# Optimization experiments

Hardware: AMD Instinct MI355X
Metric: run time of the kernel (lower is better)

Reference implementation:

```python
import jax, jax.numpy as jnp
import numpy as np

N_NODES = 100000
N_EDGES = 1600000
D_IN = 128
D_HID = 128


def _sage_conv(x, edge_index, w_l, b_l, w_r):
    """PyG SAGEConv (aggr='mean'): lin_l(mean_j x_j) + lin_r(x_i).
    lin_l has bias, lin_r does not."""
    src, dst = edge_index[0], edge_index[1]
    n = x.shape[0]
    msgs = x[src]                                   # [E, D] gather
    agg = jax.ops.segment_sum(msgs, dst, num_segments=n)        # [N, D]
    cnt = jax.ops.segment_sum(jnp.ones((src.shape[0], 1), x.dtype), dst,
                              num_segments=n)                   # [N, 1]
    mean = agg / jnp.maximum(cnt, 1.0)
    return mean @ w_l.T + b_l + x @ w_r.T


def setup_inputs() -> dict:
    key = jax.random.key(0)
    ks = jax.random.split(key, 7)
    x = jax.random.normal(ks[0], (N_NODES, D_IN), dtype=jnp.float32)
    edge_index = jax.random.randint(ks[1], (2, N_EDGES), 0, N_NODES, dtype=jnp.int64)
    s = 1.0 / np.sqrt(D_IN)
    w1_l = jax.random.uniform(ks[2], (D_HID, D_IN), jnp.float32, -s, s)
    b1_l = jnp.zeros((D_HID,), jnp.float32)
    w1_r = jax.random.uniform(ks[3], (D_HID, D_IN), jnp.float32, -s, s)
    s2 = 1.0 / np.sqrt(D_HID)
    w2_l = jax.random.uniform(ks[4], (1, D_HID), jnp.float32, -s2, s2)
    b2_l = jnp.zeros((1,), jnp.float32)
    w2_r = jax.random.uniform(ks[5], (1, D_HID), jnp.float32, -s2, s2)
    return {"x": x, "edge_index": edge_index,
            "w1_l": w1_l, "b1_l": b1_l, "w1_r": w1_r,
            "w2_l": w2_l, "b2_l": b2_l, "w2_r": w2_r}


def reference(x, edge_index, w1_l, b1_l, w1_r, w2_l, b2_l, w2_r):
    h = _sage_conv(x, edge_index, w1_l, b1_l, w1_r)          # [N, hidden]
    out = jax.nn.relu(h)
    out = _sage_conv(out, edge_index, w2_l, b2_l, w2_r)      # [N, 1]
    out = jax.nn.sigmoid(out)
    return (out, h)
```

## Files before the change

kernel.cpp:

```cpp
#include <hip/hip_runtime.h>
#include <hip/hip_bf16.h>

#define D   128
#define CAP 64

typedef __bf16 v8bf __attribute__((ext_vector_type(8)));
typedef float  v4f  __attribute__((ext_vector_type(4)));

__device__ __forceinline__ unsigned f2bf(float f) {
    unsigned u = __float_as_uint(f);
    return (u + 0x7fffu + ((u >> 16) & 1u)) >> 16;
}
__device__ __forceinline__ float bf2f_lo(unsigned v) { return __uint_as_float(v << 16); }
__device__ __forceinline__ float bf2f_hi(unsigned v) { return __uint_as_float(v & 0xffff0000u); }

__global__ void detect_k(const unsigned* __restrict__ e32, int sample, int* __restrict__ flag) {
    __shared__ int nz;
    if (threadIdx.x == 0) nz = 0;
    __syncthreads();
    int c = 0;
    for (int j = 0; j < 4; ++j) {
        int i = threadIdx.x * 4 + j;
        if (i < sample && e32[2 * i + 1] != 0u) c++;
    }
    if (c) atomicAdd(&nz, c);
    __syncthreads();
    if (threadIdx.x == 0) *flag = (nz == 0) ? 1 : 0;
}

__device__ __forceinline__ void load_edge(const void* edge, int use64, int E, int e,
                                          int& src, int& dst) {
    if (use64) {
        src = (int)((const long long*)edge)[e];
        dst = (int)((const long long*)edge)[E + e];
    } else {
        src = ((const int*)edge)[e];
        dst = ((const int*)edge)[E + e];
    }
}


__global__ __launch_bounds__(256) void xcast_k(
    const float* __restrict__ x, short* __restrict__ axm, int N)
{
    int gid = blockIdx.x * 256 + threadIdx.x;
    int g = gid >> 6, cp = gid & 63;
    if (g >= N) return;
    float2 v = *(const float2*)&x[(size_t)g * D + cp * 2];
    unsigned packed = f2bf(v.x) | (f2bf(v.y) << 16);
    *(unsigned*)&axm[(size_t)g * 256 + 128 + cp * 2] = packed;
}

__global__ __launch_bounds__(256) void build2_k(
    const void* __restrict__ edge, int* __restrict__ deg,
    int* __restrict__ slots, const int* __restrict__ flag, int E)
{
    int e0 = (blockIdx.x * 256 + threadIdx.x) * 2;
    const int use64 = *flag;
#pragma unroll
    for (int t = 0; t < 2; ++t) {
        int e = e0 + t;
        if (e < E) {
            int src, dst;
            load_edge(edge, use64, E, e, src, dst);
            int c = atomicAdd(&deg[dst], 1);
            if (c < CAP) slots[dst * CAP + c] = src;
        }
    }
}

__global__ __launch_bounds__(256) void agg_bf_k(
    short* axm, const int* __restrict__ slots,
    const int* __restrict__ deg, int N)
{
    int gw = (blockIdx.x * 256 + threadIdx.x) >> 6;
    int lane = threadIdx.x & 63;
    if (gw >= N) return;
    int dg = deg[gw];
    int n = min(dg, CAP);
    const int* sl = &slots[gw * CAP];
    float a0x = 0, a0y = 0, a1x = 0, a1y = 0, a2x = 0, a2y = 0, a3x = 0, a3y = 0;
    int j = 0;
    for (; j + 3 < n; j += 4) {
        int s0 = sl[j], s1 = sl[j + 1], s2 = sl[j + 2], s3 = sl[j + 3];
        unsigned v0 = *(const unsigned*)&axm[(size_t)s0 * 256 + 128 + lane * 2];
        unsigned v1 = *(const unsigned*)&axm[(size_t)s1 * 256 + 128 + lane * 2];
        unsigned v2 = *(const unsigned*)&axm[(size_t)s2 * 256 + 128 + lane * 2];
        unsigned v3 = *(const unsigned*)&axm[(size_t)s3 * 256 + 128 + lane * 2];
        a0x += bf2f_lo(v0); a0y += bf2f_hi(v0);
        a1x += bf2f_lo(v1); a1y += bf2f_hi(v1);
        a2x += bf2f_lo(v2); a2y += bf2f_hi(v2);
        a3x += bf2f_lo(v3); a3y += bf2f_hi(v3);
    }
    for (; j < n; ++j) {
        unsigned v0 = *(const unsigned*)&axm[(size_t)sl[j] * 256 + 128 + lane * 2];
        a0x += bf2f_lo(v0); a0y += bf2f_hi(v0);
    }
    float inv = 1.0f / fmaxf((float)dg, 1.0f);
    float mx = (a0x + a1x + a2x + a3x) * inv;
    float my = (a0y + a1y + a2y + a3y) * inv;
    *(unsigned*)&axm[(size_t)gw * 256 + lane * 2] = f2bf(mx) | (f2bf(my) << 16);
}

__global__ __launch_bounds__(256) void prep_bfrag_k(
    const float* __restrict__ w1l, const float* __restrict__ w1r,
    short* __restrict__ bfrag)
{
    int flat = blockIdx.x * 256 + threadIdx.x;
    int kt = flat >> 9, nt = (flat >> 6) & 7, lane = flat & 63;
    int c  = nt * 16 + (lane & 15);
    int k0 = kt * 32 + (lane >> 4) * 8;
    short out[8];
#pragma unroll
    for (int j = 0; j < 8; ++j) {
        int kk = k0 + j;
        float v = (kk < 128) ? w1l[c * 128 + kk] : w1r[c * 128 + (kk - 128)];
        out[j] = (short)f2bf(v);
    }
    *(uint4*)&bfrag[(size_t)flat * 8] = *(uint4*)out;
}

__global__ __launch_bounds__(256) void gemm_mfma_k(
    const short* axm, const short* __restrict__ bfrag,
    const float* __restrict__ b1,
    const float* __restrict__ w2l, const float* __restrict__ w2r,
    float* h, float* __restrict__ p, float* __restrict__ q, int N)
{
    __shared__ short sA[64 * 256];
    const int tid = threadIdx.x;
    const int row0 = blockIdx.x * 64;

#pragma unroll
    for (int i = 0; i < 8; ++i) {
        int cg = i * 256 + tid;
        int r = cg >> 5, c = cg & 31;
        int g = row0 + r;
        uint4 v = make_uint4(0u, 0u, 0u, 0u);
        if (g < N) v = *(const uint4*)&axm[(size_t)g * 256 + c * 8];
        int lb = r * 512 + ((c * 16) ^ ((r & 7) << 4));
        *(uint4*)((char*)sA + lb) = v;
    }
    __syncthreads();

    const int w    = tid >> 6;
    const int lane = tid & 63;
    const int col  = lane & 15;
    const int kg   = lane >> 4;

    v4f acc[8];
#pragma unroll
    for (int nt = 0; nt < 8; ++nt) {
        float bv = b1[nt * 16 + col];
        acc[nt] = (v4f){bv, bv, bv, bv};
    }

    const int arow  = w * 16 + col;
    const int abase = arow * 512;
    const int axor  = (arow & 7) << 4;

#pragma unroll
    for (int kt = 0; kt < 8; ++kt) {
        int chunk = kt * 4 + kg;
        v8bf a = *(const v8bf*)((const char*)sA + abase + ((chunk * 16) ^ axor));
#pragma unroll
        for (int nt = 0; nt < 8; ++nt) {
            v8bf b = *(const v8bf*)&bfrag[(size_t)(((kt * 8 + nt) << 6) + lane) * 8];
            acc[nt] = __builtin_amdgcn_mfma_f32_16x16x32_bf16(a, b, acc[nt], 0, 0, 0);
        }
    }

    float pp[4] = {0, 0, 0, 0}, qq[4] = {0, 0, 0, 0};
#pragma unroll
    for (int nt = 0; nt < 8; ++nt) {
        float w2lv = w2l[nt * 16 + col];
        float w2rv = w2r[nt * 16 + col];
#pragma unroll
        for (int r = 0; r < 4; ++r) {
            int g = row0 + w * 16 + kg * 4 + r;
            float hv = acc[nt][r];
            if (g < N) h[(size_t)g * D + nt * 16 + col] = hv;
            float rl = fmaxf(hv, 0.f);
            pp[r] += rl * w2lv;
            qq[r] += rl * w2rv;
        }
    }
#pragma unroll
    for (int r = 0; r < 4; ++r) {
#pragma unroll
        for (int m = 8; m >= 1; m >>= 1) {
            pp[r] += __shfl_xor(pp[r], m, 64);
            qq[r] += __shfl_xor(qq[r], m, 64);
        }
    }
    if (col == 0) {
#pragma unroll
        for (int r = 0; r < 4; ++r) {
            int g = row0 + w * 16 + kg * 4 + r;
            if (g < N) { p[g] = pp[r]; q[g] = qq[r]; }
        }
    }
}

__global__ __launch_bounds__(256) void final3_k(
    const float* __restrict__ p, const float* __restrict__ q,
    const int* __restrict__ slots, const int* __restrict__ deg,
    const float* __restrict__ b2, float* __restrict__ out, int N)
{
    int gw = (blockIdx.x * 256 + threadIdx.x) >> 6;
    int lane = threadIdx.x & 63;
    if (gw >= N) return;
    int dg = deg[gw];
    int n = min(dg, CAP);
    float s = 0.f;
    if (lane < n) s = p[slots[gw * CAP + lane]];
#pragma unroll
    for (int m = 32; m >= 1; m >>= 1) s += __shfl_xor(s, m, 64);
    if (lane == 0) {
        float v = s / fmaxf((float)dg, 1.0f) + b2[0] + q[gw];
        out[gw] = 1.0f / (1.0f + expf(-v));
    }
}

__global__ __launch_bounds__(256) void hist_k(
    const void* __restrict__ edge, int* __restrict__ deg,
    const int* __restrict__ flag, int E)
{
    int e = blockIdx.x * 256 + threadIdx.x;
    if (e >= E) return;
    int src, dst;
    load_edge(edge, *flag, E, e, src, dst);
    atomicAdd(&deg[dst], 1);
}

__global__ __launch_bounds__(256) void scan1_k(const int* __restrict__ deg,
                                               int* __restrict__ bsum, int N) {
    __shared__ int ts[256];
    int base = blockIdx.x * 1024;
    int tid = threadIdx.x;
    int s = 0;
#pragma unroll
    for (int j = 0; j < 4; ++j) {
        int i = base + tid * 4 + j;
        if (i < N) s += deg[i];
    }
    ts[tid] = s;
    __syncthreads();
    for (int st = 128; st > 0; st >>= 1) {
        if (tid < st) ts[tid] += ts[tid + st];
        __syncthreads();
    }
    if (tid == 0) bsum[blockIdx.x] = ts[0];
}

__global__ void scan2_k(int* __restrict__ bsum, int nb, int* __restrict__ offsets, int N) {
    if (threadIdx.x == 0 && blockIdx.x == 0) {
        int run = 0;
        for (int b = 0; b < nb; ++b) { int t = bsum[b]; bsum[b] = run; run += t; }
        offsets[N] = run;
    }
}

__global__ __launch_bounds__(256) void scan3_k(
    const int* __restrict__ deg, const int* __restrict__ bsum,
    int* __restrict__ offsets, int* __restrict__ cursor, int N)
{
    __shared__ int ts[256];
    int base = blockIdx.x * 1024;
    int tid = threadIdx.x;
    int v[4];
    int s = 0;
#pragma unroll
    for (int j = 0; j < 4; ++j) {
        int i = base + tid * 4 + j;
        v[j] = (i < N) ? deg[i] : 0;
        s += v[j];
    }
    ts[tid] = s;
    __syncthreads();
    for (int st = 1; st < 256; st <<= 1) {
        int t = (tid >= st) ? ts[tid - st] : 0;
        __syncthreads();
        ts[tid] += t;
        __syncthreads();
    }
    int excl = ts[tid] - s + bsum[blockIdx.x];
#pragma unroll
    for (int j = 0; j < 4; ++j) {
        int i = base + tid * 4 + j;
        if (i < N) { offsets[i] = excl; cursor[i] = excl; excl += v[j]; }
    }
}

__global__ __launch_bounds__(256) void build_k(
    const void* __restrict__ edge, int* __restrict__ cursor,
    int* __restrict__ sorted_src, const int* __restrict__ flag, int E)
{
    int e = blockIdx.x * 256 + threadIdx.x;
    if (e >= E) return;
    int src, dst;
    load_edge(edge, *flag, E, e, src, dst);
    int pos = atomicAdd(&cursor[dst], 1);
    sorted_src[pos] = src;
}

__global__ void transpose_k(const float* __restrict__ w1l, const float* __restrict__ w1r,
                            float* __restrict__ wlT, float* __restrict__ wrT) {
    int idx = blockIdx.x * 256 + threadIdx.x;
    int k = idx >> 7, c = idx & 127;
    wlT[idx] = w1l[c * 128 + k];
    wrT[idx] = w1r[c * 128 + k];
}

__global__ __launch_bounds__(256) void agg_mean_k(
    const float* __restrict__ x,
    const int* __restrict__ sorted_src, const int* __restrict__ offsets,
    float* __restrict__ mean_out, int N)
{
    int gw = (blockIdx.x * 256 + threadIdx.x) >> 6;
    int lane = threadIdx.x & 63;
    if (gw >= N) return;
    int o0 = offsets[gw], o1 = offsets[gw + 1];
    int col = lane * 2;
    float2 a0 = {0.f, 0.f}, a1 = {0.f, 0.f}, a2 = {0.f, 0.f}, a3 = {0.f, 0.f};
    int j = o0;
    for (; j + 3 < o1; j += 4) {
        int s0 = sorted_src[j], s1 = sorted_src[j + 1];
        int s2 = sorted_src[j + 2], s3 = sorted_src[j + 3];
        float2 v0 = *(const float2*)&x[s0 * D + col];
        float2 v1 = *(const float2*)&x[s1 * D + col];
        float2 v2 = *(const float2*)&x[s2 * D + col];
        float2 v3 = *(const float2*)&x[s3 * D + col];
        a0.x += v0.x; a0.y += v0.y;
        a1.x += v1.x; a1.y += v1.y;
        a2.x += v2.x; a2.y += v2.y;
        a3.x += v3.x; a3.y += v3.y;
    }
    for (; j < o1; ++j) {
        float2 v0 = *(const float2*)&x[sorted_src[j] * D + col];
        a0.x += v0.x; a0.y += v0.y;
    }
    float inv = 1.0f / fmaxf((float)(o1 - o0), 1.0f);
    float2 m;
    m.x = (a0.x + a1.x + a2.x + a3.x) * inv;
    m.y = (a0.y + a1.y + a2.y + a3.y) * inv;
    *(float2*)&mean_out[gw * D + col] = m;
}

__global__ __launch_bounds__(256) void gemm_k(
    const float* __restrict__ x, float* hmean,
    const float* __restrict__ wlT, const float* __restrict__ wrT,
    const float* __restrict__ b1,
    const float* __restrict__ w2l, const float* __restrict__ w2r,
    float* __restrict__ p, float* __restrict__ q, int N)
{
    __shared__ float sm[64][D];
    __shared__ float sx[64][D];
    const int tid = threadIdx.x;
    const int row0 = blockIdx.x * 64;
#pragma unroll
    for (int i = 0; i < 8; ++i) {
        int idx = i * 256 + tid;
        int r  = idx >> 5;
        int c4 = (idx & 31) * 4;
        int g = row0 + r;
        float4 xv = {0.f, 0.f, 0.f, 0.f}, mv = {0.f, 0.f, 0.f, 0.f};
        if (g < N) {
            xv = *(const float4*)&x[g * D + c4];
            mv = *(const float4*)&hmean[g * D + c4];
        }
        *(float4*)&sx[r][c4] = xv;
        *(float4*)&sm[r][c4] = mv;
    }
    __syncthreads();
    const int tc = tid & 31;
    const int tr = tid >> 5;
    float acc[8][4];
#pragma unroll
    for (int r = 0; r < 8; ++r)
#pragma unroll
        for (int c = 0; c < 4; ++c) acc[r][c] = 0.f;
    for (int kk0 = 0; kk0 < D; kk0 += 4) {
        float wl[4][4], wr_[4][4];
#pragma unroll
        for (int kk = 0; kk < 4; ++kk) {
            *(float4*)wl[kk]  = *(const float4*)&wlT[(kk0 + kk) * D + tc * 4];
            *(float4*)wr_[kk] = *(const float4*)&wrT[(kk0 + kk) * D + tc * 4];
        }
#pragma unroll
        for (int r = 0; r < 8; ++r) {
            float4 mv4 = *(const float4*)&sm[tr * 8 + r][kk0];
            float4 xv4 = *(const float4*)&sx[tr * 8 + r][kk0];
            float m[4]  = {mv4.x, mv4.y, mv4.z, mv4.w};
            float xv[4] = {xv4.x, xv4.y, xv4.z, xv4.w};
#pragma unroll
            for (int c = 0; c < 4; ++c) {
                float a = acc[r][c];
#pragma unroll
                for (int kk = 0; kk < 4; ++kk)
                    a += m[kk] * wl[kk][c] + xv[kk] * wr_[kk][c];
                acc[r][c] = a;
            }
        }
    }
    float w2lv[4], w2rv[4], b1v[4];
#pragma unroll
    for (int c = 0; c < 4; ++c) {
        int colc = tc * 4 + c;
        w2lv[c] = w2l[colc];
        w2rv[c] = w2r[colc];
        b1v[c]  = b1[colc];
    }
#pragma unroll
    for (int r = 0; r < 8; ++r) {
        int g = row0 + tr * 8 + r;
        float hv[4];
        float pp = 0.f, qq = 0.f;
#pragma unroll
        for (int c = 0; c < 4; ++c) {
            hv[c] = acc[r][c] + b1v[c];
            float rl = fmaxf(hv[c], 0.f);
            pp += rl * w2lv[c];
            qq += rl * w2rv[c];
        }
        if (g < N) {
            float4 st = {hv[0], hv[1], hv[2], hv[3]};
            *(float4*)&hmean[g * D + tc * 4] = st;
        }
#pragma unroll
        for (int m = 16; m >= 1; m >>= 1) {
            pp += __shfl_xor(pp, m, 64);
            qq += __shfl_xor(qq, m, 64);
        }
        if (tc == 0 && g < N) { p[g] = pp; q[g] = qq; }
    }
}

__global__ __launch_bounds__(256) void scatter2_k(
    const void* __restrict__ edge, const float* __restrict__ p,
    float* __restrict__ pagg, const int* __restrict__ flag, int E)
{
    int e = blockIdx.x * 256 + threadIdx.x;
    if (e >= E) return;
    int src, dst;
    load_edge(edge, *flag, E, e, src, dst);
    atomicAdd(&pagg[dst], p[src]);
}

__global__ __launch_bounds__(256) void final2_k(
    const float* __restrict__ pagg, const int* __restrict__ deg,
    const float* __restrict__ q, const float* __restrict__ b2,
    float* __restrict__ out, int N)
{
    int i = blockIdx.x * 256 + threadIdx.x;
    if (i >= N) return;
    float dg = (float)deg[i];
    float s = pagg[i] / fmaxf(dg, 1.0f) + b2[0] + q[i];
    out[i] = 1.0f / (1.0f + expf(-s));
}

extern "C" void kernel_launch(void* const* d_in, const int* in_sizes, int n_in,
                              void* d_out, int out_size, void* d_ws, size_t ws_size,
                              hipStream_t stream) {
    const float* x    = (const float*)d_in[0];
    const void*  edge = d_in[1];
    const float* w1l  = (const float*)d_in[2];
    const float* b1   = (const float*)d_in[3];
    const float* w1r  = (const float*)d_in[4];
    const float* w2l  = (const float*)d_in[5];
    const float* b2   = (const float*)d_in[6];
    const float* w2r  = (const float*)d_in[7];

    const int N = in_sizes[0] / D;
    const int E = in_sizes[1] / 2;

    float* out = (float*)d_out;
    float* h   = (float*)d_out + N;

    size_t needA = (size_t)N * (CAP + 3) * 4 + 65536 + 4096;

    if (ws_size >= needA) {
        int*   slots = (int*)d_ws;
        int*   deg   = slots + (size_t)N * CAP;
        float* p     = (float*)(deg + N);
        float* q     = p + N;
        uintptr_t ba = ((uintptr_t)(q + N) + 15) & ~(uintptr_t)15;
        short* bfrag = (short*)ba;
        int*   flag  = (int*)(bfrag + 32768);
        short* axm   = (short*)h;

        hipMemsetAsync(deg, 0, (size_t)N * sizeof(int), stream);
        detect_k<<<1, 256, 0, stream>>>((const unsigned*)edge, 1024, flag);
        prep_bfrag_k<<<16, 256, 0, stream>>>(w1l, w1r, bfrag);
        xcast_k<<<(N * 64 + 255) / 256, 256, 0, stream>>>(x, axm, N);

        build2_k<<<(E / 2 + 255) / 256, 256, 0, stream>>>(edge, deg, slots, flag, E);
        agg_bf_k<<<(N * 64 + 255) / 256, 256, 0, stream>>>(axm, slots, deg, N);
        gemm_mfma_k<<<(N + 63) / 64, 256, 0, stream>>>(axm, bfrag, b1, w2l, w2r,
                                                       h, p, q, N);
        final3_k<<<(N * 64 + 255) / 256, 256, 0, stream>>>(p, q, slots, deg, b2, out, N);
    } else {
        int*   deg     = (int*)d_ws;
        float* pagg    = (float*)(deg + N);
        int*   offsets = (int*)(pagg + N);
        int*   cursor  = offsets + N + 1;
        float* p       = (float*)(cursor + N);
        float* q       = p + N;
        float* wlT     = q + N;
        float* wrT     = wlT + D * D;
        int*   bsum    = (int*)(wrT + D * D);
        int*   flag    = bsum + 128;
        int*   ssrc    = flag + 1;
        int nb = (N + 1023) / 1024;

        hipMemsetAsync(deg, 0, (size_t)2 * N * sizeof(int), stream);
        detect_k<<<1, 256, 0, stream>>>((const unsigned*)edge, 1024, flag);
        transpose_k<<<(D * D) / 256, 256, 0, stream>>>(w1l, w1r, wlT, wrT);

        hist_k<<<(E + 255) / 256, 256, 0, stream>>>(edge, deg, flag, E);
        scan1_k<<<nb, 256, 0, stream>>>(deg, bsum, N);
        scan2_k<<<1, 64, 0, stream>>>(bsum, nb, offsets, N);
        scan3_k<<<nb, 256, 0, stream>>>(deg, bsum, offsets, cursor, N);
        build_k<<<(E + 255) / 256, 256, 0, stream>>>(edge, cursor, ssrc, flag, E);

        agg_mean_k<<<(N * 64 + 255) / 256, 256, 0, stream>>>(x, ssrc, offsets, h, N);
        gemm_k<<<(N + 63) / 64, 256, 0, stream>>>(x, h, wlT, wrT, b1, w2l, w2r,
                                                  p, q, N);
        scatter2_k<<<(E + 255) / 256, 256, 0, stream>>>(edge, p, pagg, flag, E);
        final2_k<<<(N + 255) / 256, 256, 0, stream>>>(pagg, deg, q, b2, out, N);
    }
}
```

Before: 359.6 us.

## Fuse x cast, weight prep and edge bucketing into one launch; widen gather unroll

Merges the bf16 cast of x, the MFMA weight-fragment prep and the edge bucketing into one kernel that picks its role by block index. The three independent jobs can then overlap, and two launch gaps go away. The x cast now uses 16-byte vector loads and stores, and the edge loop handles four edges per thread. The aggregation kernel unrolls the neighbour gather to 8 with int4 slot loads and more accumulators, giving more loads in flight at the cost of extra registers; the int4 slot loads rely on 16-byte slot alignment, which holds because CAP is a multiple of 4.

New measurement: 339.8 us. 1.06x faster.

```diff
diff --git a/kernel.cpp b/kernel.cpp
--- a/kernel.cpp
+++ b/kernel.cpp
@@ -40,31 +40,53 @@
 }
 
 
-__global__ __launch_bounds__(256) void xcast_k(
-    const float* __restrict__ x, short* __restrict__ axm, int N)
-{
-    int gid = blockIdx.x * 256 + threadIdx.x;
-    int g = gid >> 6, cp = gid & 63;
-    if (g >= N) return;
-    float2 v = *(const float2*)&x[(size_t)g * D + cp * 2];
-    unsigned packed = f2bf(v.x) | (f2bf(v.y) << 16);
-    *(unsigned*)&axm[(size_t)g * 256 + 128 + cp * 2] = packed;
-}
-
-__global__ __launch_bounds__(256) void build2_k(
-    const void* __restrict__ edge, int* __restrict__ deg,
-    int* __restrict__ slots, const int* __restrict__ flag, int E)
-{
-    int e0 = (blockIdx.x * 256 + threadIdx.x) * 2;
-    const int use64 = *flag;
-#pragma unroll
-    for (int t = 0; t < 2; ++t) {
-        int e = e0 + t;
-        if (e < E) {
-            int src, dst;
-            load_edge(edge, use64, E, e, src, dst);
-            int c = atomicAdd(&deg[dst], 1);
-            if (c < CAP) slots[dst * CAP + c] = src;
+__global__ __launch_bounds__(256) void stage1_k(
+    const float* __restrict__ x, const void* __restrict__ edge,
+    const float* __restrict__ w1l, const float* __restrict__ w1r,
+    short* __restrict__ axm, short* __restrict__ bfrag,
+    int* __restrict__ deg, int* __restrict__ slots,
+    const int* __restrict__ flag, int N, int E, int XB, int PB)
+{
+    const int b = blockIdx.x, tid = threadIdx.x;
+    if (b < XB) {
+        int gid = b * 256 + tid;
+        int g = gid >> 4, part = gid & 15;
+        if (g < N) {
+            const float* xr = &x[(size_t)g * D + part * 8];
+            float4 v0 = *(const float4*)xr;
+            float4 v1 = *(const float4*)(xr + 4);
+            uint4 st;
+            st.x = f2bf(v0.x) | (f2bf(v0.y) << 16);
+            st.y = f2bf(v0.z) | (f2bf(v0.w) << 16);
+            st.z = f2bf(v1.x) | (f2bf(v1.y) << 16);
+            st.w = f2bf(v1.z) | (f2bf(v1.w) << 16);
+            *(uint4*)&axm[(size_t)g * 256 + 128 + part * 8] = st;
+        }
+    } else if (b < XB + PB) {
+        int flat = (b - XB) * 256 + tid;
+        int kt = flat >> 9, nt = (flat >> 6) & 7, lane = flat & 63;
+        int c  = nt * 16 + (lane & 15);
+        int k0 = kt * 32 + (lane >> 4) * 8;
+        short out[8];
+#pragma unroll
+        for (int j = 0; j < 8; ++j) {
+            int kk = k0 + j;
+            float v = (kk < 128) ? w1l[c * 128 + kk] : w1r[c * 128 + (kk - 128)];
+            out[j] = (short)f2bf(v);
+        }
+        *(uint4*)&bfrag[(size_t)flat * 8] = *(uint4*)out;
+    } else {
+        int base = ((b - XB - PB) * 256 + tid) * 4;
+        const int use64 = *flag;
+#pragma unroll
+        for (int t = 0; t < 4; ++t) {
+            int e = base + t;
+            if (e < E) {
+                int src, dst;
+                load_edge(edge, use64, E, e, src, dst);
+                int c = atomicAdd(&deg[dst], 1);
+                if (c < CAP) slots[dst * CAP + c] = src;
+            }
         }
     }
 }
@@ -80,44 +102,48 @@
     int n = min(dg, CAP);
     const int* sl = &slots[gw * CAP];
     float a0x = 0, a0y = 0, a1x = 0, a1y = 0, a2x = 0, a2y = 0, a3x = 0, a3y = 0;
+    float a4x = 0, a4y = 0, a5x = 0, a5y = 0, a6x = 0, a6y = 0, a7x = 0, a7y = 0;
     int j = 0;
-    for (; j + 3 < n; j += 4) {
-        int s0 = sl[j], s1 = sl[j + 1], s2 = sl[j + 2], s3 = sl[j + 3];
-        unsigned v0 = *(const unsigned*)&axm[(size_t)s0 * 256 + 128 + lane * 2];
-        unsigned v1 = *(const unsigned*)&axm[(size_t)s1 * 256 + 128 + lane * 2];
-        unsigned v2 = *(const unsigned*)&axm[(size_t)s2 * 256 + 128 + lane * 2];
-        unsigned v3 = *(const unsigned*)&axm[(size_t)s3 * 256 + 128 + lane * 2];
+    for (; j + 7 < n; j += 8) {
+        int4 qa = *(const int4*)&sl[j];
+        int4 qb = *(const int4*)&sl[j + 4];
+        unsigned v0 = *(const unsigned*)&axm[(size_t)qa.x * 256 + 128 + lane * 2];
+        unsigned v1 = *(const unsigned*)&axm[(size_t)qa.y * 256 + 128 + lane * 2];
+        unsigned v2 = *(const unsigned*)&axm[(size_t)qa.z * 256 + 128 + lane * 2];
+        unsigned v3 = *(const unsigned*)&axm[(size_t)qa.w * 256 + 128 + lane * 2];
+        unsigned v4 = *(const unsigned*)&axm[(size_t)qb.x * 256 + 128 + lane * 2];
+        unsigned v5 = *(const unsigned*)&axm[(size_t)qb.y * 256 + 128 + lane * 2];
+        unsigned v6 = *(const unsigned*)&axm[(size_t)qb.z * 256 + 128 + lane * 2];
+        unsigned v7 = *(const unsigned*)&axm[(size_t)qb.w * 256 + 128 + lane * 2];
         a0x += bf2f_lo(v0); a0y += bf2f_hi(v0);
         a1x += bf2f_lo(v1); a1y += bf2f_hi(v1);
         a2x += bf2f_lo(v2); a2y += bf2f_hi(v2);
         a3x += bf2f_lo(v3); a3y += bf2f_hi(v3);
+        a4x += bf2f_lo(v4); a4y += bf2f_hi(v4);
+        a5x += bf2f_lo(v5); a5y += bf2f_hi(v5);
+        a6x += bf2f_lo(v6); a6y += bf2f_hi(v6);
+        a7x += bf2f_lo(v7); a7y += bf2f_hi(v7);
+    }
+    if (j + 3 < n) {
+        int4 qa = *(const int4*)&sl[j];
+        unsigned v0 = *(const unsigned*)&axm[(size_t)qa.x * 256 + 128 + lane * 2];
+        unsigned v1 = *(const unsigned*)&axm[(size_t)qa.y * 256 + 128 + lane * 2];
+        unsigned v2 = *(const unsigned*)&axm[(size_t)qa.z * 256 + 128 + lane * 2];
+        unsigned v3 = *(const unsigned*)&axm[(size_t)qa.w * 256 + 128 + lane * 2];
+        a0x += bf2f_lo(v0); a0y += bf2f_hi(v0);
+        a1x += bf2f_lo(v1); a1y += bf2f_hi(v1);
+        a2x += bf2f_lo(v2); a2y += bf2f_hi(v2);
+        a3x += bf2f_lo(v3); a3y += bf2f_hi(v3);
+        j += 4;
     }
     for (; j < n; ++j) {
         unsigned v0 = *(const unsigned*)&axm[(size_t)sl[j] * 256 + 128 + lane * 2];
         a0x += bf2f_lo(v0); a0y += bf2f_hi(v0);
     }
     float inv = 1.0f / fmaxf((float)dg, 1.0f);
-    float mx = (a0x + a1x + a2x + a3x) * inv;
-    float my = (a0y + a1y + a2y + a3y) * inv;
+    float mx = (((a0x + a1x) + (a2x + a3x)) + ((a4x + a5x) + (a6x + a7x))) * inv;
+    float my = (((a0y + a1y) + (a2y + a3y)) + ((a4y + a5y) + (a6y + a7y))) * inv;
     *(unsigned*)&axm[(size_t)gw * 256 + lane * 2] = f2bf(mx) | (f2bf(my) << 16);
-}
-
-__global__ __launch_bounds__(256) void prep_bfrag_k(
-    const float* __restrict__ w1l, const float* __restrict__ w1r,
-    short* __restrict__ bfrag)
-{
-    int flat = blockIdx.x * 256 + threadIdx.x;
-    int kt = flat >> 9, nt = (flat >> 6) & 7, lane = flat & 63;
-    int c  = nt * 16 + (lane & 15);
-    int k0 = kt * 32 + (lane >> 4) * 8;
-    short out[8];
-#pragma unroll
-    for (int j = 0; j < 8; ++j) {
-        int kk = k0 + j;
-        float v = (kk < 128) ? w1l[c * 128 + kk] : w1r[c * 128 + (kk - 128)];
-        out[j] = (short)f2bf(v);
-    }
-    *(uint4*)&bfrag[(size_t)flat * 8] = *(uint4*)out;
 }
 
 __global__ __launch_bounds__(256) void gemm_mfma_k(
@@ -490,10 +516,13 @@
 
         hipMemsetAsync(deg, 0, (size_t)N * sizeof(int), stream);
         detect_k<<<1, 256, 0, stream>>>((const unsigned*)edge, 1024, flag);
-        prep_bfrag_k<<<16, 256, 0, stream>>>(w1l, w1r, bfrag);
-        xcast_k<<<(N * 64 + 255) / 256, 256, 0, stream>>>(x, axm, N);
-
-        build2_k<<<(E / 2 + 255) / 256, 256, 0, stream>>>(edge, deg, slots, flag, E);
+
+        int XB = (N * 16 + 255) / 256;
+        int PB = 16;
+        int BB = (E / 4 + 255) / 256;
+        stage1_k<<<XB + PB + BB, 256, 0, stream>>>(x, edge, w1l, w1r, axm, bfrag,
+                                                   deg, slots, flag, N, E, XB, PB);
+
         agg_bf_k<<<(N * 64 + 255) / 256, 256, 0, stream>>>(axm, slots, deg, N);
         gemm_mfma_k<<<(N + 63) / 64, 256, 0, stream>>>(axm, bfrag, b1, w2l, w2r,
                                                        h, p, q, N);
```
